# Optimization experiments

Hardware: AMD Instinct MI355X
Metric: run time of the kernel (lower is better)

The kernel has to match this reference:

```python
import jax, jax.numpy as jnp
import numpy as np

B, D, N, H = 2, 512, 2048, 8
DK = D // H
EPS = 1e-5


def conv1x1(x, w, b):
    # kernel-size-1 Conv1d == channel-mixing GEMM: (o,i) x (b,i,n) -> (b,o,n)
    return jnp.einsum('oi,bin->bon', w, x) + b[None, :, None]


def setup_inputs() -> dict:
    key = jax.random.key(0)
    ks = jax.random.split(key, 20)
    s = 0.02
    return {
        'init_query': jax.random.normal(ks[0], (B, D, N), jnp.float32),
        'key_t': jax.random.normal(ks[1], (B, D, N), jnp.float32),
        'value': jax.random.normal(ks[2], (B, D, N), jnp.float32),
        'mask': jax.random.randint(ks[3], (B, 1, N, N), 0, 2, jnp.int32),
        'Wq': jax.random.normal(ks[4], (D, D), jnp.float32) * s,
        'bq': jax.random.normal(ks[5], (D,), jnp.float32) * s,
        'Wk': jax.random.normal(ks[6], (D, D), jnp.float32) * s,
        'bk': jax.random.normal(ks[7], (D,), jnp.float32) * s,
        'Wv': jax.random.normal(ks[8], (D, D), jnp.float32) * s,
        'bv': jax.random.normal(ks[9], (D,), jnp.float32) * s,
        'Wm': jax.random.normal(ks[10], (D, D), jnp.float32) * s,
        'bm': jax.random.normal(ks[11], (D,), jnp.float32) * s,
        'W1': jax.random.normal(ks[12], (2 * D, 2 * D), jnp.float32) * s,
        'b1': jax.random.normal(ks[13], (2 * D,), jnp.float32) * s,
        'gamma': jnp.ones((2 * D,), jnp.float32),
        'beta': jnp.zeros((2 * D,), jnp.float32),
        'rmean': jax.random.normal(ks[14], (2 * D,), jnp.float32) * s,
        'rvar': jnp.abs(jax.random.normal(ks[15], (2 * D,), jnp.float32)) * 0.1 + 0.5,
        'W2': jax.random.normal(ks[16], (D, 2 * D), jnp.float32) * s,
        'b2': jnp.zeros((D,), jnp.float32),  # nn.init.constant_(bias, 0.0)
    }


def reference(init_query, key_t, value, mask, Wq, bq, Wk, bk, Wv, bv, Wm, bm,
              W1, b1, gamma, beta, rmean, rvar, W2, b2):
    # projections, split channels into (d_k, n_heads) exactly like torch .view
    q = conv1x1(init_query, Wq, bq).reshape(B, DK, H, N)
    k = conv1x1(key_t, Wk, bk).reshape(B, DK, H, N)
    v = conv1x1(value, Wv, bv).reshape(B, DK, H, N)
    scores = jnp.einsum('bdhn,bdhm->bhnm', q, k) / jnp.sqrt(jnp.float32(DK))
    scores = jnp.where(mask == 0, jnp.float32(-1e9), scores)
    attn = jax.nn.softmax(scores, axis=-1)
    x = jnp.einsum('bhnm,bdhm->bdhn', attn, v).reshape(B, D, N)
    x = conv1x1(x, Wm, bm)
    x = jnp.concatenate([x, init_query], axis=1)  # (B, 2D, N)
    h = conv1x1(x, W1, b1)
    # BatchNorm1d (inference mode with running stats) + ReLU
    h = (h - rmean[None, :, None]) * (gamma / jnp.sqrt(rvar + EPS))[None, :, None] + beta[None, :, None]
    h = jax.nn.relu(h)
    return conv1x1(h, W2, b2)
```

## Files before the change

### kernel.cpp

```cpp
#include <hip/hip_runtime.h>

typedef unsigned short u16;
typedef unsigned int u32;
typedef unsigned long long u64;
typedef long long i64;
typedef __bf16 bf16x8 __attribute__((ext_vector_type(8)));
typedef u16 u16x8 __attribute__((ext_vector_type(8)));
typedef float f32x4 __attribute__((ext_vector_type(4)));
typedef float f32x16 __attribute__((ext_vector_type(16)));

#define DEV __device__ __forceinline__

constexpr int BB = 2, DD = 512, NN = 2048, HH = 8, DKc = 64, D2 = 1024;

constexpr float QSC = 0.125f * 1.44269504088896340736f;

constexpr i64 MB = 1048576;
constexpr i64 OFF_CAT = 0;
constexpr i64 OFF_XKT = 8 * MB;
constexpr i64 OFF_XVT = 12 * MB;
constexpr i64 OFF_QH  = 16 * MB;
constexpr i64 OFF_KH  = 20 * MB;
constexpr i64 OFF_VT  = 24 * MB;
constexpr i64 OFF_HT  = 28 * MB;
constexpr i64 OFF_OP  = 36 * MB;
constexpr i64 OFF_LP  = 68 * MB;
constexpr i64 OFF_WQP = 69 * MB;
constexpr i64 OFF_WKP = 69 * MB + 524288;
constexpr i64 OFF_WVP = 69 * MB + 1048576;
constexpr i64 OFF_WMT = 69 * MB + 1572864;
constexpr i64 OFF_W1A = 71 * MB;
constexpr i64 OFF_W1C = 72 * MB;
constexpr i64 OFF_W2B = 74 * MB;
constexpr i64 OFF_BQP = 75 * MB;
constexpr i64 OFF_BKP = 75 * MB + 2048;
constexpr i64 OFF_BVP = 75 * MB + 4096;
constexpr i64 OFF_BNA = 75 * MB + 8192;
constexpr i64 OFF_BNC = 75 * MB + 12288;
constexpr i64 OFF_MSK = 76 * MB;

DEV u16 f2bf(float f) {
  u32 u = __float_as_uint(f);
  u = u + 0x7FFFu + ((u >> 16) & 1u);
  return (u16)(u >> 16);
}

DEV float bf2f(u16 u) { return __uint_as_float(((u32)u) << 16); }
DEV float bf2f32(u32 u) { return __uint_as_float(u << 16); }

DEV u32 packbf(float lo, float hi) {
  return __builtin_amdgcn_perm(__float_as_uint(hi), __float_as_uint(lo), 0x07060302u);
}

DEV float fexp2(float x) {
#if __has_builtin(__builtin_amdgcn_exp2f)
  return __builtin_amdgcn_exp2f(x);
#else
  return exp2f(x);
#endif
}

DEV bf16x8 ldfrag(const u16* p) {
  bf16x8 v;
  __builtin_memcpy(&v, __builtin_assume_aligned(p, 16), 16);
  return v;
}

DEV bf16x8 ldfrag2(const u16* p0, const u16* p1) {
  bf16x8 v;
  __builtin_memcpy(&v, __builtin_assume_aligned(p0, 8), 8);
  __builtin_memcpy((char*)&v + 8, __builtin_assume_aligned(p1, 8), 8);
  return v;
}

DEV bf16x8 ones8() {
  u16x8 u = {0x3F80, 0x3F80, 0x3F80, 0x3F80, 0x3F80, 0x3F80, 0x3F80, 0x3F80};
  bf16x8 v;
  __builtin_memcpy(&v, &u, 16);
  return v;
}

DEV void gload16(const void* g, void* lds) {
  __builtin_amdgcn_global_load_lds((__attribute__((address_space(1))) void*)g,
                                   (__attribute__((address_space(3))) void*)lds, 16, 0, 0);
}

DEV f32x4 mfma16(bf16x8 a, bf16x8 b, f32x4 c) {
  return __builtin_amdgcn_mfma_f32_16x16x32_bf16(a, b, c, 0, 0, 0);
}

DEV f32x16 mfma32(bf16x8 a, bf16x8 b, f32x16 c) {
  return __builtin_amdgcn_mfma_f32_32x32x16_bf16(a, b, c, 0, 0, 0);
}

__global__ __launch_bounds__(256) void prep_all(
    const float* __restrict__ Wq, const float* __restrict__ Wk, const float* __restrict__ Wv,
    const float* __restrict__ Wm, const float* __restrict__ W1, const float* __restrict__ W2,
    const float* __restrict__ bq, const float* __restrict__ bk, const float* __restrict__ bv,
    const float* __restrict__ bm, const float* __restrict__ b1, const float* __restrict__ gamma_,
    const float* __restrict__ beta_, const float* __restrict__ rmean,
    const float* __restrict__ rvar, const int* __restrict__ mask,
    const float* __restrict__ iq, const float* __restrict__ kt, const float* __restrict__ vv,
    u16* __restrict__ wqp, u16* __restrict__ wkp, u16* __restrict__ wvp, u16* __restrict__ wmt,
    u16* __restrict__ w1a, u16* __restrict__ w1c, u16* __restrict__ w2b,
    float* __restrict__ bqp, float* __restrict__ bkp, float* __restrict__ bvp,
    float* __restrict__ bna, float* __restrict__ bnc, u32* __restrict__ mw,
    u16* __restrict__ cat, u16* __restrict__ xkt, u16* __restrict__ xvt) {
  __shared__ float tile[32][33];
  const int blk = blockIdx.x, t = threadIdx.x;
  if (blk < 768) {
    const int which = blk >> 8, lb = blk & 255;
    const float* W = which == 0 ? Wq : (which == 1 ? Wk : Wv);
    u16* dst = which == 0 ? wqp : (which == 1 ? wkp : wvp);
    for (int e = lb * 256 + t; e < 262144; e += 65536) {
      int op = e >> 9, i = e & 511;
      int dk = op & 63, h = op >> 6;
      dst[e] = f2bf(W[(dk * 8 + h) * 512 + i]);
    }
  } else if (blk < 1024) {
    const int lb = blk - 768;
    for (int e = lb * 256 + t; e < 262144; e += 65536) {
      int cp = e >> 9, o = e & 511;
      int dk = cp & 63, h = cp >> 6;
      wmt[e] = f2bf(Wm[o * 512 + dk * 8 + h]);
    }
  } else if (blk < 1280) {
    const int lb = blk - 1024;
    for (int e = lb * 256 + t; e < 524288; e += 65536) {
      int row = e >> 9, o = e & 511;
      w1a[e] = f2bf(W1[(i64)row * 1024 + o]);
    }
  } else if (blk < 1536) {
    const int lb = blk - 1280;
    for (int e = lb * 256 + t; e < 524288; e += 65536) {
      int row = e >> 9, j = e & 511;
      w1c[(i64)row * 1024 + 512 + j] = f2bf(W1[(i64)row * 1024 + 512 + j]);
    }
  } else if (blk < 1792) {
    const int lb = blk - 1536;
    for (int e = lb * 256 + t; e < 524288; e += 65536) w2b[e] = f2bf(W2[e]);
  } else if (blk < 1808) {
    __shared__ float sm[4][64];
    const int base = (blk - 1792) * 64;
    const int el = t & 63, oq = t >> 6;
    const float* wrow = W1 + (i64)(base + el) * 1024 + oq * 128;
    const float* bmq = bm + oq * 128;
    float s = 0.f;
#pragma unroll 8
    for (int j = 0; j < 128; j += 4) {
      float4 x = *(const float4*)(wrow + j);
      float4 y = *(const float4*)(bmq + j);
      s += x.x * y.x + x.y * y.y + x.z * y.z + x.w * y.w;
    }
    sm[oq][el] = s;
    __syncthreads();
    if (t < 64) {
      int e = base + t;
      float a = gamma_[e] * rsqrtf(rvar[e] + 1e-5f);
      bna[e] = a;
      bnc[e] = (b1[e] - rmean[e]) * a + beta_[e] + a * (sm[0][t] + sm[1][t] + sm[2][t] + sm[3][t]);
    }
  } else if (blk == 1808) {
    for (int e = t; e < 512; e += 256) {
      int src = (e & 63) * 8 + (e >> 6);
      bqp[e] = bq[src]; bkp[e] = bk[src]; bvp[e] = bv[src];
    }
  } else if (blk < 2833) {
    const int tid = (blk - 1809) * 256 + t;
    const i64 base = (i64)tid * 32;
    const int4* mp = (const int4*)(mask + base);
    u32 word = 0;
#pragma unroll
    for (int j = 0; j < 8; ++j) {
      int4 x = mp[j];
      u32 nib = (x.x != 0 ? 1u : 0u) | (x.y != 0 ? 2u : 0u) | (x.z != 0 ? 4u : 0u) |
                (x.w != 0 ? 8u : 0u);
      word |= nib << (j * 4);
    }
    mw[tid] = word;
  } else {
    const int idx = blk - 2833;
    const int bx = idx & 63, by = (idx >> 6) & 15, bz = idx >> 10;
    const int tensor = bz >> 1, b = bz & 1;
    const float* src = (tensor == 0 ? iq : (tensor == 1 ? kt : vv)) + (i64)b * DD * NN;
    u16* dst; i64 ldd; int coff;
    if (tensor == 0)      { dst = cat + (i64)b * NN * D2; ldd = D2; coff = DD; }
    else if (tensor == 1) { dst = xkt + (i64)b * NN * DD; ldd = DD; coff = 0; }
    else                  { dst = xvt + (i64)b * NN * DD; ldd = DD; coff = 0; }
    const int x0 = bx * 32, y0 = by * 32;
    const int col = t & 31, rg = t >> 5;
#pragma unroll
    for (int i = 0; i < 4; ++i) {
      int row = rg + i * 8;
      tile[row][col] = src[(i64)(y0 + row) * NN + x0 + col];
    }
    __syncthreads();
    const int dp = t & 15, rbase = t >> 4;
    u32* dst32 = (u32*)dst;
    const i64 ldw = ldd >> 1;
    const int cw = (coff + y0) >> 1;
#pragma unroll
    for (int i = 0; i < 2; ++i) {
      int rr = rbase + i * 16;
      dst32[(i64)(x0 + rr) * ldw + cw + dp] = packbf(tile[2 * dp][rr], tile[2 * dp + 1][rr]);
    }
  }
}

template <int AM, int AN>
DEV void gemm_core(const u16* __restrict__ A, i64 lda, const u16* __restrict__ Bp, i64 ldb,
                   int K, u16* As, u16* Bs, f32x4 (&acc)[AM][AN]) {
  constexpr int BM = AM * 32, BN = AN * 32;
  const int t = threadIdx.x, w = t >> 6, l = t & 63, quad = l >> 4, l15 = l & 15;
  const int wm = (w >> 1) * AM * 16, wn = (w & 1) * AN * 16;
  for (int kk = 0; kk < K; kk += 64) {
    __syncthreads();
#pragma unroll
    for (int j = 0; j < BM / 32; ++j) {
      int ch = j * 256 + w * 64 + l, r = ch >> 3, c = ch & 7;
      gload16(A + (i64)r * lda + kk + ((c ^ (r & 7)) << 3), As + (j * 256 + w * 64) * 8);
    }
#pragma unroll
    for (int j = 0; j < BN / 32; ++j) {
      int ch = j * 256 + w * 64 + l, r = ch >> 3, c = ch & 7;
      gload16(Bp + (i64)r * ldb + kk + ((c ^ (r & 7)) << 3), Bs + (j * 256 + w * 64) * 8);
    }
    __syncthreads();
#pragma unroll
    for (int kc = 0; kc < 2; ++kc) {
      const int sw = ((kc * 4 + quad) ^ (l15 & 7)) << 3;
      bf16x8 af[AM], bfr[AN];
#pragma unroll
      for (int i = 0; i < AM; ++i) af[i] = ldfrag(&As[(wm + i * 16 + l15) * 64 + sw]);
#pragma unroll
      for (int j = 0; j < AN; ++j) bfr[j] = ldfrag(&Bs[(wn + j * 16 + l15) * 64 + sw]);
#pragma unroll
      for (int i = 0; i < AM; ++i)
#pragma unroll
        for (int j = 0; j < AN; ++j) acc[i][j] = mfma16(af[i], bfr[j], acc[i][j]);
    }
  }
}

__global__ __launch_bounds__(256) void qkv_gemm(const u16* __restrict__ cat,
                                                const u16* __restrict__ xkt,
                                                const u16* __restrict__ xvt,
                                                const u16* __restrict__ wqp,
                                                const u16* __restrict__ wkp,
                                                const u16* __restrict__ wvp,
                                                const u16* __restrict__ w1a,
                                                const u16* __restrict__ wmt,
                                                const float* __restrict__ bqp,
                                                const float* __restrict__ bkp,
                                                const float* __restrict__ bvp,
                                                u16* __restrict__ qh, u16* __restrict__ kh,
                                                u16* __restrict__ vt, u16* __restrict__ w1c) {
  __shared__ __align__(16) u16 As[128 * 64];
  __shared__ __align__(16) u16 Bs[64 * 64];
  const int z = blockIdx.z, b = z & 1;
  const int op = (z == 6) ? 3 : (z >> 1);
  const int t = threadIdx.x, w = t >> 6, l = t & 63, quad = l >> 4, l15 = l & 15;
  const int wm = (w >> 1) * 64, wn = (w & 1) * 32;
  int mx, ny;
  const u16 *A, *Bp;
  i64 lda, ldb;
  if (op < 2) {
    mx = blockIdx.x; ny = blockIdx.y;
    A = (op == 0 ? cat + DD : xkt);
    lda = (op == 0 ? D2 : DD);
    A += (i64)b * NN * lda + (i64)mx * 128 * lda;
    Bp = (op == 0 ? wqp : wkp) + (i64)ny * 64 * DD;
    ldb = DD;
  } else if (op == 2) {
    int f = blockIdx.x * 8 + blockIdx.y;
    mx = f >> 5; ny = f & 31;
    A = wvp + (i64)mx * 128 * DD; lda = DD;
    Bp = xvt + (i64)b * NN * DD + (i64)ny * 64 * DD; ldb = DD;
  } else {
    if (blockIdx.x >= 8) return;
    mx = blockIdx.x; ny = blockIdx.y;
    A = w1a + (i64)mx * 128 * DD; lda = DD;
    Bp = wmt + (i64)ny * 64 * DD; ldb = DD;
  }
  f32x4 acc[4][2] = {};
  gemm_core<4, 2>(A, lda, Bp, ldb, DD, As, Bs, acc);

  const int rowBase = mx * 128 + wm + quad * 4;
  const int colBase = ny * 64 + wn + l15;
  if (op < 2) {
    const float* bias = (op == 0 ? bqp : bkp);
    const float sc = (op == 0 ? QSC : 1.f);
    u16* dst = (op == 0 ? qh : kh) + (i64)b * HH * NN * DKc;
#pragma unroll
    for (int j = 0; j < 2; ++j) {
      const int col = colBase + j * 16;
      const float cA = bias[col];
#pragma unroll
      for (int i = 0; i < 4; ++i)
#pragma unroll
        for (int r = 0; r < 4; ++r) {
          const int row = rowBase + i * 16 + r;
          dst[(i64)(col >> 6) * (NN * 64) + (i64)row * 64 + (col & 63)] =
              f2bf((acc[i][j][r] + cA) * sc);
        }
    }
  } else if (op == 2) {
    u16* dst = vt + (i64)b * HH * DKc * NN;
#pragma unroll
    for (int j = 0; j < 2; ++j) {
      const int col = colBase + j * 16;
#pragma unroll
      for (int i = 0; i < 4; ++i)
#pragma unroll
        for (int r = 0; r < 4; ++r) {
          const int row = rowBase + i * 16 + r;
          dst[(i64)row * NN + col] = f2bf(acc[i][j][r] + bvp[row]);
        }
    }
  } else {
#pragma unroll
    for (int j = 0; j < 2; ++j) {
      const int col = colBase + j * 16;
#pragma unroll
      for (int i = 0; i < 4; ++i)
#pragma unroll
        for (int r = 0; r < 4; ++r) {
          const int row = rowBase + i * 16 + r;
          w1c[(i64)row * D2 + col] = f2bf(acc[i][j][r]);
        }
    }
  }
}

struct GArgs {
  const u16* A; i64 lda, sAb;
  const u16* B; i64 ldb, sBb;
  void* C; i64 ldc, sCb;
  const float* p1; const float* p2;
  int K;
};

template <int MODE, int AM, int AN, int SWZ>
__global__ __launch_bounds__(256) void gemm_bt(GArgs g) {
  __shared__ __align__(16) u16 As[AM * 32 * 64];
  __shared__ __align__(16) u16 Bs[AN * 32 * 64];
  const int t = threadIdx.x, w = t >> 6, l = t & 63, quad = l >> 4, l15 = l & 15;
  const int wm = (w >> 1) * AM * 16, wn = (w & 1) * AN * 16;
  int bx = blockIdx.x, by = blockIdx.y, bz = blockIdx.z;
  if (SWZ == 1) {
    const int i = bx + (by << 3) + (bz << 8);
    const int slot = i & 7, jj = i >> 3;
    by = slot + ((jj & 3) << 3);
    const int j2 = jj >> 2;
    bx = j2 & 7;
    bz = j2 >> 3;
  }
  const u16* A = g.A + (i64)bz * g.sAb + (i64)bx * (AM * 32) * g.lda;
  const u16* Bp = g.B + (i64)bz * g.sBb + (i64)by * (AN * 32) * g.ldb;
  f32x4 acc[AM][AN] = {};
  gemm_core<AM, AN>(A, g.lda, Bp, g.ldb, g.K, As, Bs, acc);

  const int rowBase = bx * (AM * 32) + wm + quad * 4;
  const int colBase = by * (AN * 32) + wn + l15;
#pragma unroll
  for (int j = 0; j < AN; ++j) {
    const int col = colBase + j * 16;
    float cA = 0.f, cB = 0.f;
    if (MODE == 3) { cA = g.p1[col]; cB = g.p2[col]; }
#pragma unroll
    for (int i = 0; i < AM; ++i) {
#pragma unroll
      for (int r = 0; r < 4; ++r) {
        const int row = rowBase + i * 16 + r;
        float v = acc[i][j][r];
        if (MODE == 3) {
          float x = v * cA + cB;
          ((u16*)g.C + (i64)bz * g.sCb)[(i64)row * g.ldc + col] = f2bf(x > 0.f ? x : 0.f);
        } else {
          ((float*)g.C + (i64)bz * g.sCb)[(i64)row * g.ldc + col] = v + g.p1[row];
        }
      }
    }
  }
}

__global__ __launch_bounds__(256) void flash_attn(const u16* __restrict__ Qh,
                                                  const u16* __restrict__ Kh,
                                                  const u16* __restrict__ Vt,
                                                  const u64* __restrict__ MW64,
                                                  u16* __restrict__ Opart,
                                                  float* __restrict__ Lp) {
  __shared__ __align__(16) u16 Ks[64 * 64];
  __shared__ __align__(16) u16 Vs[64 * 64];
  const int t = threadIdx.x, w = t >> 6, l = t & 63, l31 = l & 31, lh = l >> 5;
  const int flat = blockIdx.x;
  const int h = flat & 7;
  const int j = flat >> 3;
  const int nt = j & 15, zz = j >> 4;
  const int b = zz >> 2, sp = zz & 3;
  const int n = nt * 128 + w * 32 + l31;
  const u16* Qb = Qh + ((i64)(b * HH + h) * NN + nt * 128 + w * 32) * 64;
  const u16* Kb = Kh + (i64)(b * HH + h) * NN * 64;
  const u16* Vb = Vt + (i64)(b * HH + h) * 64 * NN;
  const u64* mwp = MW64 + (i64)(b * NN + n) * 32;
  const bf16x8 ONE = ones8();
  bf16x8 qf[4];
#pragma unroll
  for (int kc = 0; kc < 4; ++kc)
    __builtin_memcpy(&qf[kc], Qb + (i64)l31 * 64 + kc * 16 + lh * 8, 16);

  f32x16 oacc0 = {}, oacc1 = {}, lacc = {};
  for (int mt = sp * 8; mt < sp * 8 + 8; ++mt) {
    __syncthreads();
#pragma unroll
    for (int j2 = 0; j2 < 2; ++j2) {
      int ch = j2 * 256 + t, r = ch >> 3, c = ch & 7;
      gload16(Kb + (i64)(mt * 64 + r) * 64 + ((c ^ (r & 7)) << 3), &Ks[ch * 8]);
      gload16(Vb + (i64)r * NN + mt * 64 + ((c ^ (r & 7)) << 3), &Vs[ch * 8]);
    }
    __syncthreads();
    f32x16 s0 = {}, s1 = {};
#pragma unroll
    for (int kc = 0; kc < 4; ++kc) {
      const int sw = l31 & 7;
      bf16x8 k0 = ldfrag(&Ks[l31 * 64 + (((kc * 2 + lh) ^ sw) << 3)]);
      bf16x8 k1 = ldfrag(&Ks[(32 + l31) * 64 + (((kc * 2 + lh) ^ sw) << 3)]);
      s0 = mfma32(k0, qf[kc], s0);
      s1 = mfma32(k1, qf[kc], s1);
    }
    const u64 mrow = mwp[mt];
    u32 pw[16];
#pragma unroll
    for (int k = 0; k < 8; ++k) {
      const int kvb = ((2 * k) & 3) + 8 * ((2 * k) >> 2) + 4 * lh;
      u64 sh = mrow >> kvb;
      u32 mA = (((u32)sh & 1u) | (((u32)sh & 2u) << 15)) * 0xFFFFu;
      u32 shh = (u32)(sh >> 32);
      u32 mB = ((shh & 1u) | ((shh & 2u) << 15)) * 0xFFFFu;
      pw[k] = packbf(fexp2(s0[2 * k]), fexp2(s0[2 * k + 1])) & mA;
      pw[8 + k] = packbf(fexp2(s1[2 * k]), fexp2(s1[2 * k + 1])) & mB;
    }
    bf16x8 pf[4];
#pragma unroll
    for (int c = 0; c < 4; ++c) __builtin_memcpy(&pf[c], &pw[c * 4], 16);
#pragma unroll
    for (int c = 0; c < 4; ++c) lacc = mfma32(ONE, pf[c], lacc);
#pragma unroll
    for (int c = 0; c < 4; ++c) {
      const int sw0 = l31 & 7;
      const u16* r0 = &Vs[l31 * 64];
      const u16* r1 = &Vs[(32 + l31) * 64];
      bf16x8 v0 = ldfrag2(r0 + (((2 * c) ^ sw0) << 3) + lh * 4,
                          r0 + (((2 * c + 1) ^ sw0) << 3) + lh * 4);
      bf16x8 v1 = ldfrag2(r1 + (((2 * c) ^ sw0) << 3) + lh * 4,
                          r1 + (((2 * c + 1) ^ sw0) << 3) + lh * 4);
      oacc0 = mfma32(v0, pf[c], oacc0);
      oacc1 = mfma32(v1, pf[c], oacc1);
    }
  }
  u16* OpT = Opart + ((i64)((sp * BB + b) * HH + h) * 64) * NN;
#pragma unroll
  for (int r = 0; r < 16; ++r) {
    const int d0 = (r & 3) + 8 * (r >> 2) + 4 * lh;
    OpT[(i64)d0 * NN + n] = f2bf(oacc0[r]);
    OpT[(i64)(d0 + 32) * NN + n] = f2bf(oacc1[r]);
  }
  if (lh == 0) Lp[((i64)(sp * BB + b) * HH + h) * NN + n] = lacc[0];
}

__global__ __launch_bounds__(256) void combine(const u16* __restrict__ Opart,
                                               const float* __restrict__ Lp,
                                               u16* __restrict__ cat) {
  __shared__ float lt[128 * 65];
  const int t = threadIdx.x;
  const int nt = blockIdx.x, bh = blockIdx.y;
  const int b = bh >> 3, h = bh & 7;
  const int n0 = nt * 128;
  const i64 sstride = (i64)BB * HH * 64 * NN;
  const u16* Ob = Opart + ((i64)(b * HH + h) * 64) * NN;
#pragma unroll
  for (int i = 0; i < 16; ++i) {
    const int idx = i * 256 + t;
    const int d = idx >> 6, np = idx & 63;
    float sa = 0.f, sb = 0.f;
#pragma unroll
    for (int s = 0; s < 4; ++s) {
      u32 v;
      __builtin_memcpy(&v, Ob + s * sstride + (i64)d * NN + n0 + 2 * np, 4);
      sa += bf2f32(v & 0xFFFFu);
      sb += bf2f32(v >> 16);
    }
    lt[(2 * np) * 65 + d] = sa;
    lt[(2 * np + 1) * 65 + d] = sb;
  }
  __syncthreads();
  u32* catw = (u32*)cat;
#pragma unroll
  for (int i = 0; i < 16; ++i) {
    const int idx = i * 256 + t;
    const int nn = idx >> 5, dp = idx & 31;
    float lsum = 0.f;
#pragma unroll
    for (int s = 0; s < 4; ++s) lsum += Lp[((i64)(s * BB + b) * HH + h) * NN + n0 + nn];
    const float rl = __builtin_amdgcn_rcpf(lsum);
    u32 pv = packbf(lt[nn * 65 + 2 * dp] * rl, lt[nn * 65 + 2 * dp + 1] * rl);
    catw[((i64)b * NN + n0 + nn) * (D2 / 2) + h * 32 + dp] = pv;
  }
}

extern "C" void kernel_launch(void* const* d_in, const int* in_sizes, int n_in,
                              void* d_out, int out_size, void* d_ws, size_t ws_size,
                              hipStream_t stream) {
  (void)in_sizes; (void)n_in; (void)out_size; (void)ws_size;
  const float* iq    = (const float*)d_in[0];
  const float* kt    = (const float*)d_in[1];
  const float* vv    = (const float*)d_in[2];
  const int*   mask  = (const int*)d_in[3];
  const float* Wq    = (const float*)d_in[4];
  const float* bq    = (const float*)d_in[5];
  const float* Wk    = (const float*)d_in[6];
  const float* bk    = (const float*)d_in[7];
  const float* Wv    = (const float*)d_in[8];
  const float* bv    = (const float*)d_in[9];
  const float* Wm    = (const float*)d_in[10];
  const float* bm    = (const float*)d_in[11];
  const float* W1    = (const float*)d_in[12];
  const float* b1    = (const float*)d_in[13];
  const float* gamma_= (const float*)d_in[14];
  const float* beta_ = (const float*)d_in[15];
  const float* rmean = (const float*)d_in[16];
  const float* rvar  = (const float*)d_in[17];
  const float* W2    = (const float*)d_in[18];
  const float* b2    = (const float*)d_in[19];

  char* ws = (char*)d_ws;
  u16* cat = (u16*)(ws + OFF_CAT);
  u16* xkt = (u16*)(ws + OFF_XKT);
  u16* xvt = (u16*)(ws + OFF_XVT);
  u16* qh  = (u16*)(ws + OFF_QH);
  u16* kh  = (u16*)(ws + OFF_KH);
  u16* vt  = (u16*)(ws + OFF_VT);
  u16* ht  = (u16*)(ws + OFF_HT);
  u16* opart = (u16*)(ws + OFF_OP);
  float* lp  = (float*)(ws + OFF_LP);
  u16* wqp = (u16*)(ws + OFF_WQP);
  u16* wkp = (u16*)(ws + OFF_WKP);
  u16* wvp = (u16*)(ws + OFF_WVP);
  u16* wmt = (u16*)(ws + OFF_WMT);
  u16* w1a = (u16*)(ws + OFF_W1A);
  u16* w1c = (u16*)(ws + OFF_W1C);
  u16* w2b = (u16*)(ws + OFF_W2B);
  float* bqp = (float*)(ws + OFF_BQP);
  float* bkp = (float*)(ws + OFF_BKP);
  float* bvp = (float*)(ws + OFF_BVP);
  float* bna = (float*)(ws + OFF_BNA);
  float* bnc = (float*)(ws + OFF_BNC);
  u32* mw = (u32*)(ws + OFF_MSK);

  prep_all<<<8977, 256, 0, stream>>>(Wq, Wk, Wv, Wm, W1, W2, bq, bk, bv, bm, b1, gamma_, beta_,
                                     rmean, rvar, mask, iq, kt, vv, wqp, wkp, wvp, wmt, w1a, w1c,
                                     w2b, bqp, bkp, bvp, bna, bnc, mw, cat, xkt, xvt);
  qkv_gemm<<<dim3(16, 8, 7), 256, 0, stream>>>(cat, xkt, xvt, wqp, wkp, wvp, w1a, wmt,
                                               bqp, bkp, bvp, qh, kh, vt, w1c);
  flash_attn<<<1024, 256, 0, stream>>>(qh, kh, vt, (const u64*)mw, opart, lp);
  combine<<<dim3(16, 16), 256, 0, stream>>>(opart, lp, cat);
  GArgs wa{cat, D2, 0, w1c, D2, 0, ht, D2, 0, bna, bnc, D2};
  gemm_bt<3, 4, 2, 0><<<dim3(32, 16, 1), 256, 0, stream>>>(wa);
  GArgs w2a{w2b, D2, 0, ht, D2, (i64)NN * D2, d_out, NN, (i64)DD * NN, b2, nullptr, D2};
  gemm_bt<4, 2, 2, 1><<<dim3(8, 32, 2), 256, 0, stream>>>(w2a);
}
```

Before: 220.9 us.

## Double-buffer K/V tiles in flash attention and widen QKV GEMM tiles

The flash attention kernel now keeps two LDS buffers for K and V. It issues the global-to-LDS load of the next key tile before computing on the current one, so memory latency overlaps with MFMA work. The QKV GEMM switches from 128x64 to 128x128 output tiles on a flat 416-block grid, which gives more operand reuse per block and drops the idle early-return blocks. The cost is extra LDS and registers in both kernels, which may lower occupancy.

```diff
diff --git a/kernel.cpp b/kernel.cpp
--- a/kernel.cpp
+++ b/kernel.cpp
@@ -256,43 +256,53 @@
                                                 u16* __restrict__ qh, u16* __restrict__ kh,
                                                 u16* __restrict__ vt, u16* __restrict__ w1c) {
   __shared__ __align__(16) u16 As[128 * 64];
-  __shared__ __align__(16) u16 Bs[64 * 64];
-  const int z = blockIdx.z, b = z & 1;
-  const int op = (z == 6) ? 3 : (z >> 1);
+  __shared__ __align__(16) u16 Bs[128 * 64];
+  const int flat = blockIdx.x;
   const int t = threadIdx.x, w = t >> 6, l = t & 63, quad = l >> 4, l15 = l & 15;
-  const int wm = (w >> 1) * 64, wn = (w & 1) * 32;
-  int mx, ny;
+  const int wm = (w >> 1) * 64, wn = (w & 1) * 64;
+  int op, b = 0, mx, ny;
+  if (flat < 256) {
+    op = flat >> 7;
+    b = (flat >> 6) & 1;
+    const int r = flat & 63;
+    mx = r >> 2; ny = r & 3;
+  } else if (flat < 384) {
+    op = 2;
+    const int r = flat - 256;
+    b = r >> 6;
+    const int rr = r & 63;
+    mx = rr >> 4; ny = rr & 15;
+  } else {
+    op = 3;
+    const int r = flat - 384;
+    mx = r >> 2; ny = r & 3;
+  }
   const u16 *A, *Bp;
   i64 lda, ldb;
   if (op < 2) {
-    mx = blockIdx.x; ny = blockIdx.y;
     A = (op == 0 ? cat + DD : xkt);
     lda = (op == 0 ? D2 : DD);
     A += (i64)b * NN * lda + (i64)mx * 128 * lda;
-    Bp = (op == 0 ? wqp : wkp) + (i64)ny * 64 * DD;
+    Bp = (op == 0 ? wqp : wkp) + (i64)ny * 128 * DD;
     ldb = DD;
   } else if (op == 2) {
-    int f = blockIdx.x * 8 + blockIdx.y;
-    mx = f >> 5; ny = f & 31;
     A = wvp + (i64)mx * 128 * DD; lda = DD;
-    Bp = xvt + (i64)b * NN * DD + (i64)ny * 64 * DD; ldb = DD;
+    Bp = xvt + (i64)b * NN * DD + (i64)ny * 128 * DD; ldb = DD;
   } else {
-    if (blockIdx.x >= 8) return;
-    mx = blockIdx.x; ny = blockIdx.y;
     A = w1a + (i64)mx * 128 * DD; lda = DD;
-    Bp = wmt + (i64)ny * 64 * DD; ldb = DD;
-  }
-  f32x4 acc[4][2] = {};
-  gemm_core<4, 2>(A, lda, Bp, ldb, DD, As, Bs, acc);
+    Bp = wmt + (i64)ny * 128 * DD; ldb = DD;
+  }
+  f32x4 acc[4][4] = {};
+  gemm_core<4, 4>(A, lda, Bp, ldb, DD, As, Bs, acc);
 
   const int rowBase = mx * 128 + wm + quad * 4;
-  const int colBase = ny * 64 + wn + l15;
+  const int colBase = ny * 128 + wn + l15;
   if (op < 2) {
     const float* bias = (op == 0 ? bqp : bkp);
     const float sc = (op == 0 ? QSC : 1.f);
     u16* dst = (op == 0 ? qh : kh) + (i64)b * HH * NN * DKc;
 #pragma unroll
-    for (int j = 0; j < 2; ++j) {
+    for (int j = 0; j < 4; ++j) {
       const int col = colBase + j * 16;
       const float cA = bias[col];
 #pragma unroll
@@ -307,7 +317,7 @@
   } else if (op == 2) {
     u16* dst = vt + (i64)b * HH * DKc * NN;
 #pragma unroll
-    for (int j = 0; j < 2; ++j) {
+    for (int j = 0; j < 4; ++j) {
       const int col = colBase + j * 16;
 #pragma unroll
       for (int i = 0; i < 4; ++i)
@@ -319,7 +329,7 @@
     }
   } else {
 #pragma unroll
-    for (int j = 0; j < 2; ++j) {
+    for (int j = 0; j < 4; ++j) {
       const int col = colBase + j * 16;
 #pragma unroll
       for (int i = 0; i < 4; ++i)
@@ -390,8 +400,10 @@
                                                   const u64* __restrict__ MW64,
                                                   u16* __restrict__ Opart,
                                                   float* __restrict__ Lp) {
-  __shared__ __align__(16) u16 Ks[64 * 64];
-  __shared__ __align__(16) u16 Vs[64 * 64];
+  __shared__ __align__(16) u16 Ks0[64 * 64];
+  __shared__ __align__(16) u16 Ks1[64 * 64];
+  __shared__ __align__(16) u16 Vs0[64 * 64];
+  __shared__ __align__(16) u16 Vs1[64 * 64];
   const int t = threadIdx.x, w = t >> 6, l = t & 63, l31 = l & 31, lh = l >> 5;
   const int flat = blockIdx.x;
   const int h = flat & 7;
@@ -410,21 +422,23 @@
     __builtin_memcpy(&qf[kc], Qb + (i64)l31 * 64 + kc * 16 + lh * 8, 16);
 
   f32x16 oacc0 = {}, oacc1 = {}, lacc = {};
-  for (int mt = sp * 8; mt < sp * 8 + 8; ++mt) {
-    __syncthreads();
+  const int mt0 = sp * 8;
+
+  auto stage = [&](u16* Kd, u16* Vd, int mt) {
 #pragma unroll
     for (int j2 = 0; j2 < 2; ++j2) {
       int ch = j2 * 256 + t, r = ch >> 3, c = ch & 7;
-      gload16(Kb + (i64)(mt * 64 + r) * 64 + ((c ^ (r & 7)) << 3), &Ks[ch * 8]);
-      gload16(Vb + (i64)r * NN + mt * 64 + ((c ^ (r & 7)) << 3), &Vs[ch * 8]);
-    }
-    __syncthreads();
+      gload16(Kb + (i64)(mt * 64 + r) * 64 + ((c ^ (r & 7)) << 3), Kd + ch * 8);
+      gload16(Vb + (i64)r * NN + mt * 64 + ((c ^ (r & 7)) << 3), Vd + ch * 8);
+    }
+  };
+  auto compute = [&](const u16* Kc, const u16* Vc, int mt) {
     f32x16 s0 = {}, s1 = {};
 #pragma unroll
     for (int kc = 0; kc < 4; ++kc) {
       const int sw = l31 & 7;
-      bf16x8 k0 = ldfrag(&Ks[l31 * 64 + (((kc * 2 + lh) ^ sw) << 3)]);
-      bf16x8 k1 = ldfrag(&Ks[(32 + l31) * 64 + (((kc * 2 + lh) ^ sw) << 3)]);
+      bf16x8 k0 = ldfrag(&Kc[l31 * 64 + (((kc * 2 + lh) ^ sw) << 3)]);
+      bf16x8 k1 = ldfrag(&Kc[(32 + l31) * 64 + (((kc * 2 + lh) ^ sw) << 3)]);
       s0 = mfma32(k0, qf[kc], s0);
       s1 = mfma32(k1, qf[kc], s1);
     }
@@ -448,8 +462,8 @@
 #pragma unroll
     for (int c = 0; c < 4; ++c) {
       const int sw0 = l31 & 7;
-      const u16* r0 = &Vs[l31 * 64];
-      const u16* r1 = &Vs[(32 + l31) * 64];
+      const u16* r0 = &Vc[l31 * 64];
+      const u16* r1 = &Vc[(32 + l31) * 64];
       bf16x8 v0 = ldfrag2(r0 + (((2 * c) ^ sw0) << 3) + lh * 4,
                           r0 + (((2 * c + 1) ^ sw0) << 3) + lh * 4);
       bf16x8 v1 = ldfrag2(r1 + (((2 * c) ^ sw0) << 3) + lh * 4,
@@ -457,6 +471,17 @@
       oacc0 = mfma32(v0, pf[c], oacc0);
       oacc1 = mfma32(v1, pf[c], oacc1);
     }
+  };
+
+  stage(Ks0, Vs0, mt0);
+#pragma unroll
+  for (int i = 0; i < 8; i += 2) {
+    __syncthreads();
+    stage(Ks1, Vs1, mt0 + i + 1);
+    compute(Ks0, Vs0, mt0 + i);
+    __syncthreads();
+    if (i + 2 < 8) stage(Ks0, Vs0, mt0 + i + 2);
+    compute(Ks1, Vs1, mt0 + i + 1);
   }
   u16* OpT = Opart + ((i64)((sp * BB + b) * HH + h) * 64) * NN;
 #pragma unroll
@@ -560,8 +585,8 @@
   prep_all<<<8977, 256, 0, stream>>>(Wq, Wk, Wv, Wm, W1, W2, bq, bk, bv, bm, b1, gamma_, beta_,
                                      rmean, rvar, mask, iq, kt, vv, wqp, wkp, wvp, wmt, w1a, w1c,
                                      w2b, bqp, bkp, bvp, bna, bnc, mw, cat, xkt, xvt);
-  qkv_gemm<<<dim3(16, 8, 7), 256, 0, stream>>>(cat, xkt, xvt, wqp, wkp, wvp, w1a, wmt,
-                                               bqp, bkp, bvp, qh, kh, vt, w1c);
+  qkv_gemm<<<416, 256, 0, stream>>>(cat, xkt, xvt, wqp, wkp, wvp, w1a, wmt,
+                                    bqp, bkp, bvp, qh, kh, vt, w1c);
   flash_attn<<<1024, 256, 0, stream>>>(qh, kh, vt, (const u64*)mw, opart, lp);
   combine<<<dim3(16, 16), 256, 0, stream>>>(opart, lp, cat);
   GArgs wa{cat, D2, 0, w1c, D2, 0, ht, D2, 0, bna, bnc, D2};
```

Measured after the change: 218.7 us. Within noise of the previous version (-1.0%).
